# Optimization experiments

Measured on AMD Instinct MI355X. Metric: run time of the kernel, lower is better.

## Reference

```python
import jax, jax.numpy as jnp
import numpy as np

HEADS = 4
DIM_HEAD = 32
CHUNK = 1024
GROUPS = 8
EPS = 1e-5


def setup_inputs() -> dict:
    key = jax.random.key(0)
    k1, k2, k3 = jax.random.split(key, 3)
    b, dim, h, w = 8, 64, 96, 96
    inner = HEADS * DIM_HEAD  # 128
    x = jax.random.normal(k1, (b, dim, h, w), dtype=jnp.float32)
    W_qkv = jax.random.normal(k2, (3 * inner, dim), dtype=jnp.float32) * (1.0 / np.sqrt(dim))
    W_out = jax.random.normal(k3, (dim, inner), dtype=jnp.float32) * (1.0 / np.sqrt(inner))
    b_out = jnp.zeros((dim,), dtype=jnp.float32)
    gamma = jnp.ones((dim,), dtype=jnp.float32)
    beta = jnp.zeros((dim,), dtype=jnp.float32)
    return {"x": x, "W_qkv": W_qkv, "W_out": W_out, "b_out": b_out,
            "gamma": gamma, "beta": beta}


def reference(x, W_qkv, W_out, b_out, gamma, beta):
    b, c, h, w = x.shape
    n = h * w
    nch = n // CHUNK  # number of full chunks (n chosen divisible by CHUNK)
    d = DIM_HEAD
    BH = b * HEADS

    # 1x1 conv (no bias) == matmul over channel dim
    xf = x.reshape(b, c, n)
    qkv = jnp.einsum('oc,bcn->bon', W_qkv, xf)          # [b, 3*inner, n]
    q, k, v = jnp.split(qkv, 3, axis=1)                  # each [b, inner, n]

    def chunkify(t):
        # [b, inner, n] -> [BH, nch, d, CHUNK]; slicing i:i+CHUNK on last axis
        # equals reshaping n -> (nch, CHUNK) in order.
        return t.reshape(BH, d, nch, CHUNK).transpose(0, 2, 1, 3)

    qc, kc, vc = chunkify(q), chunkify(k), chunkify(v)

    qs = jax.nn.softmax(qc, axis=-1)  # softmax over chunk spatial positions
    ks = jax.nn.softmax(kc, axis=-2)  # softmax over head channels

    # context = k_chunk^T @ v_chunk : [BH, nch, CHUNK, CHUNK]
    ctx = jnp.einsum('gkdi,gkdj->gkij', ks, vc)
    # chunk_out = q_chunk @ context : [BH, nch, d, CHUNK]
    out = jnp.einsum('gkdi,gkij->gkdj', qs, ctx)

    # concat chunks back along spatial dim, reshape to image layout
    out = out.transpose(0, 2, 1, 3).reshape(b, HEADS * d, h, w)

    # to_out: 1x1 conv with bias, then GroupNorm(8, dim)
    y = jnp.einsum('oc,bchw->bohw', W_out, out) + b_out[None, :, None, None]

    yg = y.reshape(b, GROUPS, c // GROUPS, h, w)
    mu = jnp.mean(yg, axis=(2, 3, 4), keepdims=True)
    var = jnp.var(yg, axis=(2, 3, 4), keepdims=True)
    yn = ((yg - mu) * jax.lax.rsqrt(var + EPS)).reshape(b, c, h, w)
    return yn * gamma[None, :, None, None] + beta[None, :, None, None]
```

## Files before the change

kernel.cpp:

```cpp
#include <hip/hip_runtime.h>
#include <hip/hip_bf16.h>

#define N_POS 9216
#define NCHUNK 9
#define BATCH 8
#define CDIM 64
#define HEADS 4
#define EPS 1e-5f

#define NPART 16
#define PPARTS_TOT ((size_t)BATCH * NCHUNK * NPART * 4096)
#define MP_SLICE ((size_t)(BATCH * NCHUNK) * 4096)
#define WBF_BYTES ((size_t)384 * 64 * 2)

typedef __attribute__((ext_vector_type(8))) short short8;
typedef __attribute__((ext_vector_type(4))) float f32x4;

static __device__ inline unsigned pk2(float a, float b) {
    __hip_bfloat162 h2(__float2bfloat16(a), __float2bfloat16(b));
    return *reinterpret_cast<unsigned*>(&h2);
}
static __device__ inline float bf2f(short s) {
    union { unsigned u; float f; } c; c.u = ((unsigned)(unsigned short)s) << 16; return c.f;
}
static __device__ inline short8 mk8(unsigned a, unsigned b, unsigned c, unsigned d) {
    union { short8 s; unsigned u[4]; } cv;
    cv.u[0] = a; cv.u[1] = b; cv.u[2] = c; cv.u[3] = d; return cv.s;
}

__global__ __launch_bounds__(256) void wprep_kernel(const float* __restrict__ Wqkv,
        __hip_bfloat16* __restrict__ wbf, float* __restrict__ stats) {
    int i = blockIdx.x * 256 + threadIdx.x;
    if (i < 6144) {
        float4 v = ((const float4*)Wqkv)[i];
        uint2 u; u.x = pk2(v.x, v.y); u.y = pk2(v.z, v.w);
        ((uint2*)wbf)[i] = u;
    }
    if (i < 128) stats[i] = 0.f;
}

__global__ __launch_bounds__(256) void qkp_kernel(const float* __restrict__ x,
        const __hip_bfloat16* __restrict__ wbf, float* __restrict__ Pparts) {
    int bx = blockIdx.x;
    int b  = blockIdx.y;
    int ck = bx >> 4, pt = bx & 15;
    __shared__ __align__(16) __hip_bfloat16 xs[64][72];
    int t = threadIdx.x, w = t >> 6, l = t & 63;
    int l15 = l & 15, quad = l >> 4;
    int n0 = bx * 64;

    {
        int p = t & 63, cbase = (t >> 6) * 16;
        const float* xb = x + (size_t)b * CDIM * N_POS + n0 + p;
        #pragma unroll
        for (int j = 0; j < 16; j += 4) {
            float v0 = xb[(size_t)(cbase + j + 0) * N_POS];
            float v1 = xb[(size_t)(cbase + j + 1) * N_POS];
            float v2 = xb[(size_t)(cbase + j + 2) * N_POS];
            float v3 = xb[(size_t)(cbase + j + 3) * N_POS];
            uint2 u; u.x = pk2(v0, v1); u.y = pk2(v2, v3);
            *reinterpret_cast<uint2*>(&xs[p][cbase + j]) = u;
        }
    }
    __syncthreads();

    f32x4 acc[4][4];
    #pragma unroll
    for (int mt = 0; mt < 4; ++mt)
        #pragma unroll
        for (int nt = 0; nt < 4; ++nt) acc[mt][nt] = (f32x4){0.f, 0.f, 0.f, 0.f};
    #pragma unroll
    for (int ks = 0; ks < 2; ++ks) {
        int k0 = ks * 32 + quad * 8;
        short8 av[4];
        #pragma unroll
        for (int mt = 0; mt < 4; ++mt)
            av[mt] = *reinterpret_cast<const short8*>(&xs[mt * 16 + l15][k0]);
        #pragma unroll
        for (int nt = 0; nt < 4; ++nt) {
            int row = (nt < 2) ? (w * 32 + nt * 16 + l15)
                               : (128 + w * 32 + (nt - 2) * 16 + l15);
            short8 bw = *reinterpret_cast<const short8*>(wbf + (size_t)row * 64 + k0);
            #pragma unroll
            for (int mt = 0; mt < 4; ++mt)
                acc[mt][nt] = __builtin_amdgcn_mfma_f32_16x16x32_bf16(av[mt], bw, acc[mt][nt], 0, 0, 0);
        }
    }

    unsigned pk[4][4][2];
    #pragma unroll
    for (int mt = 0; mt < 4; ++mt) {
        f32x4 e2, e3;
        #pragma unroll
        for (int r = 0; r < 4; ++r) {
            float a2 = acc[mt][2][r], a3 = acc[mt][3][r];
            float m = fmaxf(a2, a3);
            m = fmaxf(m, __shfl_xor(m, 1));
            m = fmaxf(m, __shfl_xor(m, 2));
            m = fmaxf(m, __shfl_xor(m, 4));
            m = fmaxf(m, __shfl_xor(m, 8));
            float x2 = __expf(a2 - m), x3 = __expf(a3 - m);
            float s = x2 + x3;
            s += __shfl_xor(s, 1);
            s += __shfl_xor(s, 2);
            s += __shfl_xor(s, 4);
            s += __shfl_xor(s, 8);
            float is = 1.f / s;
            e2[r] = x2 * is; e3[r] = x3 * is;
        }
        pk[mt][2][0] = pk2(e2[0], e2[1]); pk[mt][2][1] = pk2(e2[2], e2[3]);
        pk[mt][3][0] = pk2(e3[0], e3[1]); pk[mt][3][1] = pk2(e3[2], e3[3]);
        pk[mt][0][0] = pk2(__expf(acc[mt][0][0]), __expf(acc[mt][0][1]));
        pk[mt][0][1] = pk2(__expf(acc[mt][0][2]), __expf(acc[mt][0][3]));
        pk[mt][1][0] = pk2(__expf(acc[mt][1][0]), __expf(acc[mt][1][1]));
        pk[mt][1][1] = pk2(__expf(acc[mt][1][2]), __expf(acc[mt][1][3]));
    }

    f32x4 pac[2][2];
    pac[0][0] = (f32x4){0,0,0,0}; pac[0][1] = (f32x4){0,0,0,0};
    pac[1][0] = (f32x4){0,0,0,0}; pac[1][1] = (f32x4){0,0,0,0};
    int srcbase = ((quad & 1) * 2) * 16 + l15;
    bool hiHalf = (quad >= 2);
    #pragma unroll
    for (int ks = 0; ks < 2; ++ks) {
        unsigned fr[4][4];
        #pragma unroll
        for (int nt = 0; nt < 4; ++nt) {
            #pragma unroll
            for (int s = 0; s < 4; ++s) {
                int src = srcbase + (s >> 1) * 16;
                unsigned lo = __shfl(pk[2 * ks][nt][s & 1], src);
                unsigned hi = __shfl(pk[2 * ks + 1][nt][s & 1], src);
                fr[nt][s] = hiHalf ? hi : lo;
            }
        }
        short8 A0 = mk8(fr[0][0], fr[0][1], fr[0][2], fr[0][3]);
        short8 A1 = mk8(fr[1][0], fr[1][1], fr[1][2], fr[1][3]);
        short8 B0 = mk8(fr[2][0], fr[2][1], fr[2][2], fr[2][3]);
        short8 B1 = mk8(fr[3][0], fr[3][1], fr[3][2], fr[3][3]);
        pac[0][0] = __builtin_amdgcn_mfma_f32_16x16x32_bf16(A0, B0, pac[0][0], 0, 0, 0);
        pac[0][1] = __builtin_amdgcn_mfma_f32_16x16x32_bf16(A0, B1, pac[0][1], 0, 0, 0);
        pac[1][0] = __builtin_amdgcn_mfma_f32_16x16x32_bf16(A1, B0, pac[1][0], 0, 0, 0);
        pac[1][1] = __builtin_amdgcn_mfma_f32_16x16x32_bf16(A1, B1, pac[1][1], 0, 0, 0);
    }
    float* Pp = Pparts + (((size_t)(b * NCHUNK + ck) * NPART + pt) * 4 + w) * 1024;
    #pragma unroll
    for (int tA = 0; tA < 2; ++tA)
        #pragma unroll
        for (int tB = 0; tB < 2; ++tB)
            #pragma unroll
            for (int r = 0; r < 4; ++r)
                Pp[(tA * 16 + quad * 4 + r) * 32 + tB * 16 + l15] = pac[tA][tB][r];
}

__global__ __launch_bounds__(256) void umat_kernel(const float* __restrict__ Wout,
        const float* __restrict__ Wqkv, const float* __restrict__ Pparts,
        float* __restrict__ Mp) {
    int ck = blockIdx.x, b = blockIdx.y, h = blockIdx.z;
    int t = threadIdx.x;
    __shared__ float Pl[32][32];
    __shared__ float iZ[32];
    __shared__ float Ul[64][33];
    __shared__ float Wvh[32][68];
    {
        const float4* P0 = (const float4*)Pparts
            + ((size_t)(b * NCHUNK + ck) * NPART) * 1024 + h * 256 + t;
        float4 s = (float4){0.f, 0.f, 0.f, 0.f};
        #pragma unroll
        for (int pt = 0; pt < NPART; ++pt) {
            float4 a = P0[pt * 1024];
            s.x += a.x; s.y += a.y; s.z += a.z; s.w += a.w;
        }
        ((float4*)Pl)[t] = s;
    }
    {
        int e = t >> 3, cq = t & 7;
        const float4* wr = (const float4*)(Wqkv + (size_t)(256 + h * 32 + e) * 64 + cq * 8);
        float4 a0 = wr[0], a1 = wr[1];
        *reinterpret_cast<float4*>(&Wvh[e][cq * 8])     = a0;
        *reinterpret_cast<float4*>(&Wvh[e][cq * 8 + 4]) = a1;
    }
    __syncthreads();
    if (t < 32) {
        float s = 0.f;
        #pragma unroll
        for (int c = 0; c < 32; ++c) s += Pl[t][c];
        iZ[t] = 1.f / s;
    }
    __syncthreads();
    int o = t & 63, wv = t >> 6;
    float wz[32];
    {
        const float4* wr = (const float4*)(Wout + (size_t)o * 128 + h * 32);
        #pragma unroll
        for (int j = 0; j < 8; ++j) {
            float4 f = wr[j];
            wz[j*4+0] = f.x * iZ[j*4+0]; wz[j*4+1] = f.y * iZ[j*4+1];
            wz[j*4+2] = f.z * iZ[j*4+2]; wz[j*4+3] = f.w * iZ[j*4+3];
        }
    }
    float ua[8];
    #pragma unroll
    for (int j = 0; j < 8; ++j) ua[j] = 0.f;
    for (int d = 0; d < 32; ++d) {
        float wd = wz[d];
        #pragma unroll
        for (int j = 0; j < 8; ++j) ua[j] += wd * Pl[d][wv * 8 + j];
    }
    #pragma unroll
    for (int j = 0; j < 8; ++j) Ul[o][wv * 8 + j] = ua[j];
    __syncthreads();

    float macc[16];
    #pragma unroll
    for (int j = 0; j < 16; ++j) macc[j] = 0.f;
    for (int e = 0; e < 32; ++e) {
        float u = Ul[o][e];
        const float4* wvp = reinterpret_cast<const float4*>(&Wvh[e][wv * 16]);
        #pragma unroll
        for (int q = 0; q < 4; ++q) {
            float4 f = wvp[q];
            macc[q*4+0] += u * f.x; macc[q*4+1] += u * f.y;
            macc[q*4+2] += u * f.z; macc[q*4+3] += u * f.w;
        }
    }
    float* mp = Mp + (size_t)h * MP_SLICE + ((size_t)(b * NCHUNK + ck)) * 4096
              + (size_t)o * 64 + wv * 16;
    #pragma unroll
    for (int q = 0; q < 4; ++q) {
        float4 f; f.x = macc[q*4+0]; f.y = macc[q*4+1]; f.z = macc[q*4+2]; f.w = macc[q*4+3];
        reinterpret_cast<float4*>(mp)[q] = f;
    }
}

__global__ __launch_bounds__(256) void y_kernel(const float* __restrict__ x,
        const float* __restrict__ Mp, const float* __restrict__ bout,
        __hip_bfloat16* __restrict__ ybf, float* __restrict__ stats) {
    int bx = blockIdx.x;
    int b  = blockIdx.y;
    int ck = bx >> 3;
    int n0 = bx * 128;
    __shared__ __align__(16) __hip_bfloat16 xs[128][72];
    __shared__ __align__(16) __hip_bfloat16 Ml[64][72];
    __shared__ float gsum[8], gsq[8];
    int t = threadIdx.x, w = t >> 6, l = t & 63;
    int l15 = l & 15, quad = l >> 4;
    if (t < 8) { gsum[t] = 0.f; gsq[t] = 0.f; }

    {
        int p = t & 127, cbase = (t >> 7) * 32;
        const float* xb = x + (size_t)b * CDIM * N_POS + n0 + p;
        #pragma unroll
        for (int j = 0; j < 32; j += 4) {
            float v0 = xb[(size_t)(cbase + j + 0) * N_POS];
            float v1 = xb[(size_t)(cbase + j + 1) * N_POS];
            float v2 = xb[(size_t)(cbase + j + 2) * N_POS];
            float v3 = xb[(size_t)(cbase + j + 3) * N_POS];
            uint2 u; u.x = pk2(v0, v1); u.y = pk2(v2, v3);
            *reinterpret_cast<uint2*>(&xs[p][cbase + j]) = u;
        }
    }
    {
        int o = t >> 2, cs = (t & 3) * 16;
        const float* mb = Mp + ((size_t)(b * NCHUNK + ck)) * 4096 + (size_t)o * 64 + cs;
        float m[16];
        #pragma unroll
        for (int q = 0; q < 4; ++q) {
            float4 f = reinterpret_cast<const float4*>(mb)[q];
            m[q*4+0] = f.x; m[q*4+1] = f.y; m[q*4+2] = f.z; m[q*4+3] = f.w;
        }
        #pragma unroll
        for (int h = 1; h < 4; ++h) {
            const float* mh = mb + h * MP_SLICE;
            #pragma unroll
            for (int q = 0; q < 4; ++q) {
                float4 f = reinterpret_cast<const float4*>(mh)[q];
                m[q*4+0] += f.x; m[q*4+1] += f.y; m[q*4+2] += f.z; m[q*4+3] += f.w;
            }
        }
        #pragma unroll
        for (int q = 0; q < 4; ++q) {
            uint2 u; u.x = pk2(m[q*4+0], m[q*4+1]); u.y = pk2(m[q*4+2], m[q*4+3]);
            *reinterpret_cast<uint2*>(&Ml[o][cs + q * 4]) = u;
        }
    }
    __syncthreads();

    int nw = w * 32;
    f32x4 acc[4][2];
    #pragma unroll
    for (int mt = 0; mt < 4; ++mt) { acc[mt][0] = (f32x4){0,0,0,0}; acc[mt][1] = (f32x4){0,0,0,0}; }
    #pragma unroll
    for (int ks = 0; ks < 2; ++ks) {
        int k0 = ks * 32 + quad * 8;
        short8 bf[2];
        #pragma unroll
        for (int nt = 0; nt < 2; ++nt)
            bf[nt] = *reinterpret_cast<const short8*>(&xs[nw + nt * 16 + l15][k0]);
        #pragma unroll
        for (int mt = 0; mt < 4; ++mt) {
            short8 af = *reinterpret_cast<const short8*>(&Ml[mt * 16 + l15][k0]);
            acc[mt][0] = __builtin_amdgcn_mfma_f32_16x16x32_bf16(af, bf[0], acc[mt][0], 0, 0, 0);
            acc[mt][1] = __builtin_amdgcn_mfma_f32_16x16x32_bf16(af, bf[1], acc[mt][1], 0, 0, 0);
        }
    }
    float gsl[4], gql[4];
    #pragma unroll
    for (int mt = 0; mt < 4; ++mt) { gsl[mt] = 0.f; gql[mt] = 0.f; }
    __hip_bfloat16* yb = ybf + (size_t)b * CDIM * N_POS;
    int nbase = n0 + nw;
    #pragma unroll
    for (int mt = 0; mt < 4; ++mt) {
        float4 bo = *reinterpret_cast<const float4*>(bout + mt * 16 + quad * 4);
        const float* bop = reinterpret_cast<const float*>(&bo);
        #pragma unroll
        for (int nt = 0; nt < 2; ++nt) {
            int n = nbase + nt * 16 + l15;
            #pragma unroll
            for (int r = 0; r < 4; ++r) {
                int o = mt * 16 + quad * 4 + r;
                float val = acc[mt][nt][r] + bop[r];
                yb[(size_t)o * N_POS + n] = __float2bfloat16(val);
                gsl[mt] += val; gql[mt] += val * val;
            }
        }
    }
    #pragma unroll
    for (int off = 16; off >= 1; off >>= 1) {
        #pragma unroll
        for (int mt = 0; mt < 4; ++mt) {
            gsl[mt] += __shfl_xor(gsl[mt], off, 64);
            gql[mt] += __shfl_xor(gql[mt], off, 64);
        }
    }
    if (l == 0 || l == 32) {
        int qh = quad >> 1;
        #pragma unroll
        for (int mt = 0; mt < 4; ++mt) {
            atomicAdd(&gsum[2 * mt + qh], gsl[mt]);
            atomicAdd(&gsq[2 * mt + qh], gql[mt]);
        }
    }
    __syncthreads();
    if (t < 8) {
        atomicAdd(&stats[(b * 8 + t) * 2],     gsum[t]);
        atomicAdd(&stats[(b * 8 + t) * 2 + 1], gsq[t]);
    }
}

__global__ __launch_bounds__(256) void gn_kernel(const __hip_bfloat16* __restrict__ ybf,
        float* __restrict__ out, const float* __restrict__ stats,
        const float* __restrict__ gamma, const float* __restrict__ beta) {
    int bc = blockIdx.y;
    int c = bc & 63, b = bc >> 6;
    int g = c >> 3;
    float s = stats[(b * 8 + g) * 2], q = stats[(b * 8 + g) * 2 + 1];
    const float invN = 1.f / (8.f * N_POS);
    float mean = s * invN;
    float var = q * invN - mean * mean;
    float sc = rsqrtf(var + EPS);
    float ga = gamma[c] * sc;
    float be = beta[c] - mean * sc * gamma[c];
    size_t base = ((size_t)b * CDIM + c) * N_POS + (size_t)(blockIdx.x * 256 + threadIdx.x) * 4;
    uint2 u = *reinterpret_cast<const uint2*>(ybf + base);
    float4 v;
    v.x = bf2f((short)(u.x & 0xffff)); v.y = bf2f((short)(u.x >> 16));
    v.z = bf2f((short)(u.y & 0xffff)); v.w = bf2f((short)(u.y >> 16));
    v.x = v.x * ga + be; v.y = v.y * ga + be; v.z = v.z * ga + be; v.w = v.w * ga + be;
    *reinterpret_cast<float4*>(out + base) = v;
}

extern "C" void kernel_launch(void* const* d_in, const int* in_sizes, int n_in,
                              void* d_out, int out_size, void* d_ws, size_t ws_size,
                              hipStream_t stream) {
    const float* x     = (const float*)d_in[0];
    const float* Wqkv  = (const float*)d_in[1];
    const float* Wout  = (const float*)d_in[2];
    const float* bout  = (const float*)d_in[3];
    const float* gamma = (const float*)d_in[4];
    const float* beta  = (const float*)d_in[5];
    float* out = (float*)d_out;

    float* stats  = (float*)d_ws;
    float* Pparts = stats + 128;
    float* Mp     = Pparts + PPARTS_TOT;
    __hip_bfloat16* wbf = (__hip_bfloat16*)(Mp + 4 * MP_SLICE);
    __hip_bfloat16* ybf = (__hip_bfloat16*)((char*)wbf + WBF_BYTES);

    wprep_kernel<<<dim3(24), 256, 0, stream>>>(Wqkv, wbf, stats);
    qkp_kernel<<<dim3(144, BATCH), 256, 0, stream>>>(x, wbf, Pparts);
    umat_kernel<<<dim3(NCHUNK, BATCH, HEADS), 256, 0, stream>>>(Wout, Wqkv, Pparts, Mp);
    y_kernel<<<dim3(72, BATCH), 256, 0, stream>>>(x, Mp, bout, ybf, stats);
    gn_kernel<<<dim3(9, 512), 256, 0, stream>>>(ybf, out, stats, gamma, beta);
}
```

Baseline: 130.9 us.

## Fuse all stages into one persistent cooperative kernel with grid syncs

Replaces the five separate launches with one cooperative persistent kernel. Each block loops over the tasks of every phase, and the phases are separated by grid-wide syncs. The weight bf16 prep kernel is dropped; weights are converted inline inside phase A. This removes launch gaps and tail effects between kernels, at the cost of grid-sync overhead, fewer blocks than the original grids, and redundant per-tile weight conversion. A fallback path with four separate kernels is kept for when the cooperative launch fails.

```diff
diff --git a/kernel.cpp b/kernel.cpp
--- a/kernel.cpp
+++ b/kernel.cpp
@@ -1,5 +1,8 @@
 #include <hip/hip_runtime.h>
+#include <hip/hip_cooperative_groups.h>
 #include <hip/hip_bf16.h>
+
+namespace cg = cooperative_groups;
 
 #define N_POS 9216
 #define NCHUNK 9
@@ -11,7 +14,6 @@
 #define NPART 16
 #define PPARTS_TOT ((size_t)BATCH * NCHUNK * NPART * 4096)
 #define MP_SLICE ((size_t)(BATCH * NCHUNK) * 4096)
-#define WBF_BYTES ((size_t)384 * 64 * 2)
 
 typedef __attribute__((ext_vector_type(8))) short short8;
 typedef __attribute__((ext_vector_type(4))) float f32x4;
@@ -28,27 +30,16 @@
     cv.u[0] = a; cv.u[1] = b; cv.u[2] = c; cv.u[3] = d; return cv.s;
 }
 
-__global__ __launch_bounds__(256) void wprep_kernel(const float* __restrict__ Wqkv,
-        __hip_bfloat16* __restrict__ wbf, float* __restrict__ stats) {
-    int i = blockIdx.x * 256 + threadIdx.x;
-    if (i < 6144) {
-        float4 v = ((const float4*)Wqkv)[i];
-        uint2 u; u.x = pk2(v.x, v.y); u.y = pk2(v.z, v.w);
-        ((uint2*)wbf)[i] = u;
-    }
-    if (i < 128) stats[i] = 0.f;
-}
-
-__global__ __launch_bounds__(256) void qkp_kernel(const float* __restrict__ x,
-        const __hip_bfloat16* __restrict__ wbf, float* __restrict__ Pparts) {
-    int bx = blockIdx.x;
-    int b  = blockIdx.y;
+static __device__ __forceinline__ void phaseA_task(int task, int t,
+        const float* __restrict__ x, const float* __restrict__ Wqkv,
+        float* __restrict__ Pparts) {
+    __shared__ __align__(16) __hip_bfloat16 xs[64][72];
+    int w = t >> 6, l = t & 63;
+    int l15 = l & 15, quad = l >> 4;
+    int bx = task % 144, b = task / 144;
     int ck = bx >> 4, pt = bx & 15;
-    __shared__ __align__(16) __hip_bfloat16 xs[64][72];
-    int t = threadIdx.x, w = t >> 6, l = t & 63;
-    int l15 = l & 15, quad = l >> 4;
     int n0 = bx * 64;
-
+    __syncthreads();
     {
         int p = t & 63, cbase = (t >> 6) * 16;
         const float* xb = x + (size_t)b * CDIM * N_POS + n0 + p;
@@ -80,10 +71,13 @@
         for (int nt = 0; nt < 4; ++nt) {
             int row = (nt < 2) ? (w * 32 + nt * 16 + l15)
                                : (128 + w * 32 + (nt - 2) * 16 + l15);
-            short8 bw = *reinterpret_cast<const short8*>(wbf + (size_t)row * 64 + k0);
+            const float4* wr = (const float4*)(Wqkv + (size_t)row * 64 + k0);
+            float4 wa = wr[0], wb = wr[1];
+            short8 bwv = mk8(pk2(wa.x, wa.y), pk2(wa.z, wa.w),
+                             pk2(wb.x, wb.y), pk2(wb.z, wb.w));
             #pragma unroll
             for (int mt = 0; mt < 4; ++mt)
-                acc[mt][nt] = __builtin_amdgcn_mfma_f32_16x16x32_bf16(av[mt], bw, acc[mt][nt], 0, 0, 0);
+                acc[mt][nt] = __builtin_amdgcn_mfma_f32_16x16x32_bf16(av[mt], bwv, acc[mt][nt], 0, 0, 0);
         }
     }
 
@@ -127,11 +121,11 @@
         #pragma unroll
         for (int nt = 0; nt < 4; ++nt) {
             #pragma unroll
-            for (int s = 0; s < 4; ++s) {
-                int src = srcbase + (s >> 1) * 16;
-                unsigned lo = __shfl(pk[2 * ks][nt][s & 1], src);
-                unsigned hi = __shfl(pk[2 * ks + 1][nt][s & 1], src);
-                fr[nt][s] = hiHalf ? hi : lo;
+            for (int sl = 0; sl < 4; ++sl) {
+                int src = srcbase + (sl >> 1) * 16;
+                unsigned lo = __shfl(pk[2 * ks][nt][sl & 1], src);
+                unsigned hi = __shfl(pk[2 * ks + 1][nt][sl & 1], src);
+                fr[nt][sl] = hiHalf ? hi : lo;
             }
         }
         short8 A0 = mk8(fr[0][0], fr[0][1], fr[0][2], fr[0][3]);
@@ -153,15 +147,15 @@
                 Pp[(tA * 16 + quad * 4 + r) * 32 + tB * 16 + l15] = pac[tA][tB][r];
 }
 
-__global__ __launch_bounds__(256) void umat_kernel(const float* __restrict__ Wout,
-        const float* __restrict__ Wqkv, const float* __restrict__ Pparts,
-        float* __restrict__ Mp) {
-    int ck = blockIdx.x, b = blockIdx.y, h = blockIdx.z;
-    int t = threadIdx.x;
+static __device__ __forceinline__ void phaseB_task(int task, int t,
+        const float* __restrict__ Wqkv, const float* __restrict__ Wout,
+        const float* __restrict__ Pparts, float* __restrict__ Mp) {
     __shared__ float Pl[32][32];
     __shared__ float iZ[32];
     __shared__ float Ul[64][33];
     __shared__ float Wvh[32][68];
+    int ck = task % 9; int r2 = task / 9; int b = r2 & 7; int h = r2 >> 3;
+    __syncthreads();
     {
         const float4* P0 = (const float4*)Pparts
             + ((size_t)(b * NCHUNK + ck) * NPART) * 1024 + h * 256 + t;
@@ -233,20 +227,20 @@
     }
 }
 
-__global__ __launch_bounds__(256) void y_kernel(const float* __restrict__ x,
-        const float* __restrict__ Mp, const float* __restrict__ bout,
-        __hip_bfloat16* __restrict__ ybf, float* __restrict__ stats) {
-    int bx = blockIdx.x;
-    int b  = blockIdx.y;
-    int ck = bx >> 3;
-    int n0 = bx * 128;
+static __device__ __forceinline__ void phaseC_task(int task, int t,
+        const float* __restrict__ x, const float* __restrict__ Mp,
+        const float* __restrict__ bout, __hip_bfloat16* __restrict__ ybf,
+        float* __restrict__ stats) {
     __shared__ __align__(16) __hip_bfloat16 xs[128][72];
     __shared__ __align__(16) __hip_bfloat16 Ml[64][72];
     __shared__ float gsum[8], gsq[8];
-    int t = threadIdx.x, w = t >> 6, l = t & 63;
+    int w = t >> 6, l = t & 63;
     int l15 = l & 15, quad = l >> 4;
+    int bx = task % 72, b = task / 72;
+    int ck = bx >> 3;
+    int n0 = bx * 128;
+    __syncthreads();
     if (t < 8) { gsum[t] = 0.f; gsq[t] = 0.f; }
-
     {
         int p = t & 127, cbase = (t >> 7) * 32;
         const float* xb = x + (size_t)b * CDIM * N_POS + n0 + p;
@@ -348,10 +342,11 @@
     }
 }
 
-__global__ __launch_bounds__(256) void gn_kernel(const __hip_bfloat16* __restrict__ ybf,
-        float* __restrict__ out, const float* __restrict__ stats,
-        const float* __restrict__ gamma, const float* __restrict__ beta) {
-    int bc = blockIdx.y;
+static __device__ __forceinline__ void phaseD_task(int task, int t,
+        const __hip_bfloat16* __restrict__ ybf, const float* __restrict__ stats,
+        const float* __restrict__ gamma, const float* __restrict__ beta,
+        float* __restrict__ out) {
+    int bx9 = task % 9; int bc = task / 9;
     int c = bc & 63, b = bc >> 6;
     int g = c >> 3;
     float s = stats[(b * 8 + g) * 2], q = stats[(b * 8 + g) * 2 + 1];
@@ -361,13 +356,61 @@
     float sc = rsqrtf(var + EPS);
     float ga = gamma[c] * sc;
     float be = beta[c] - mean * sc * gamma[c];
-    size_t base = ((size_t)b * CDIM + c) * N_POS + (size_t)(blockIdx.x * 256 + threadIdx.x) * 4;
+    size_t base = ((size_t)b * CDIM + c) * N_POS + (size_t)(bx9 * 256 + t) * 4;
     uint2 u = *reinterpret_cast<const uint2*>(ybf + base);
     float4 v;
     v.x = bf2f((short)(u.x & 0xffff)); v.y = bf2f((short)(u.x >> 16));
     v.z = bf2f((short)(u.y & 0xffff)); v.w = bf2f((short)(u.y >> 16));
     v.x = v.x * ga + be; v.y = v.y * ga + be; v.z = v.z * ga + be; v.w = v.w * ga + be;
     *reinterpret_cast<float4*>(out + base) = v;
+}
+
+__global__ __launch_bounds__(256, 2) void fused_kernel(
+        const float* __restrict__ x, const float* __restrict__ Wqkv,
+        const float* __restrict__ Wout, const float* __restrict__ bout,
+        const float* __restrict__ gamma, const float* __restrict__ beta,
+        float* __restrict__ out, float* __restrict__ stats,
+        float* __restrict__ Pparts, float* __restrict__ Mp,
+        __hip_bfloat16* __restrict__ ybf) {
+    cg::grid_group gg = cg::this_grid();
+    int t = threadIdx.x;
+    if (blockIdx.x == 0 && t < 128) stats[t] = 0.f;
+    for (int task = blockIdx.x; task < 1152; task += gridDim.x)
+        phaseA_task(task, t, x, Wqkv, Pparts);
+    __threadfence();
+    gg.sync();
+    for (int task = blockIdx.x; task < 288; task += gridDim.x)
+        phaseB_task(task, t, Wqkv, Wout, Pparts, Mp);
+    __threadfence();
+    gg.sync();
+    for (int task = blockIdx.x; task < 576; task += gridDim.x)
+        phaseC_task(task, t, x, Mp, bout, ybf, stats);
+    __threadfence();
+    gg.sync();
+    for (int task = blockIdx.x; task < 4608; task += gridDim.x)
+        phaseD_task(task, t, ybf, stats, gamma, beta, out);
+}
+
+__global__ __launch_bounds__(256) void kA(const float* __restrict__ x,
+        const float* __restrict__ Wqkv, float* __restrict__ Pparts,
+        float* __restrict__ stats) {
+    if (blockIdx.x == 0 && threadIdx.x < 128) stats[threadIdx.x] = 0.f;
+    phaseA_task(blockIdx.x, threadIdx.x, x, Wqkv, Pparts);
+}
+__global__ __launch_bounds__(256) void kB(const float* __restrict__ Wqkv,
+        const float* __restrict__ Wout, const float* __restrict__ Pparts,
+        float* __restrict__ Mp) {
+    phaseB_task(blockIdx.x, threadIdx.x, Wqkv, Wout, Pparts, Mp);
+}
+__global__ __launch_bounds__(256) void kC(const float* __restrict__ x,
+        const float* __restrict__ Mp, const float* __restrict__ bout,
+        __hip_bfloat16* __restrict__ ybf, float* __restrict__ stats) {
+    phaseC_task(blockIdx.x, threadIdx.x, x, Mp, bout, ybf, stats);
+}
+__global__ __launch_bounds__(256) void kD(const __hip_bfloat16* __restrict__ ybf,
+        const float* __restrict__ stats, const float* __restrict__ gamma,
+        const float* __restrict__ beta, float* __restrict__ out) {
+    phaseD_task(blockIdx.x, threadIdx.x, ybf, stats, gamma, beta, out);
 }
 
 extern "C" void kernel_launch(void* const* d_in, const int* in_sizes, int n_in,
@@ -384,12 +427,31 @@
     float* stats  = (float*)d_ws;
     float* Pparts = stats + 128;
     float* Mp     = Pparts + PPARTS_TOT;
-    __hip_bfloat16* wbf = (__hip_bfloat16*)(Mp + 4 * MP_SLICE);
-    __hip_bfloat16* ybf = (__hip_bfloat16*)((char*)wbf + WBF_BYTES);
-
-    wprep_kernel<<<dim3(24), 256, 0, stream>>>(Wqkv, wbf, stats);
-    qkp_kernel<<<dim3(144, BATCH), 256, 0, stream>>>(x, wbf, Pparts);
-    umat_kernel<<<dim3(NCHUNK, BATCH, HEADS), 256, 0, stream>>>(Wout, Wqkv, Pparts, Mp);
-    y_kernel<<<dim3(72, BATCH), 256, 0, stream>>>(x, Mp, bout, ybf, stats);
-    gn_kernel<<<dim3(9, 512), 256, 0, stream>>>(ybf, out, stats, gamma, beta);
-}
+    __hip_bfloat16* ybf = (__hip_bfloat16*)(Mp + 4 * MP_SLICE);
+
+    static int coopBlocks = -1;
+    if (coopBlocks < 0) {
+        int nb = 0;
+        if (hipOccupancyMaxActiveBlocksPerMultiprocessor(
+                &nb, (const void*)fused_kernel, 256, 0) != hipSuccess || nb < 1)
+            nb = 0;
+        coopBlocks = nb * 256;
+        if (coopBlocks > 512) coopBlocks = 512;
+    }
+
+    bool done = false;
+    if (coopBlocks >= 256) {
+        void* args[] = { (void*)&x, (void*)&Wqkv, (void*)&Wout, (void*)&bout,
+                         (void*)&gamma, (void*)&beta, (void*)&out, (void*)&stats,
+                         (void*)&Pparts, (void*)&Mp, (void*)&ybf };
+        if (hipLaunchCooperativeKernel((const void*)fused_kernel,
+                dim3(coopBlocks), dim3(256), args, 0, stream) == hipSuccess)
+            done = true;
+    }
+    if (!done) {
+        kA<<<dim3(1152), 256, 0, stream>>>(x, Wqkv, Pparts, stats);
+        kB<<<dim3(288),  256, 0, stream>>>(Wqkv, Wout, Pparts, Mp);
+        kC<<<dim3(576),  256, 0, stream>>>(x, Mp, bout, ybf, stats);
+        kD<<<dim3(4608), 256, 0, stream>>>(ybf, stats, gamma, beta, out);
+    }
+}
```

After: 343.0 us. 2.62x slower.

## Fuse GroupNorm into y kernel via per-batch grid barrier and drop weight prep

Applied to the files above, without the earlier changes.

Folds the GroupNorm apply into the output-projection kernel. Each batch's blocks accumulate group statistics, then spin on a per-batch atomic counter until all 72 blocks have arrived, and write normalized fp32 output straight from registers. This removes the bf16 intermediate round trip and the separate gn launch. It also drops the weight bf16 prep kernel, converting Wqkv to bf16 inline in qkp, and replaces it with a memset to clear the stats and counters. The spin barrier needs all blocks resident, so it launches cooperatively with a plain launch as fallback, which risks deadlock if blocks are not co-resident.

```diff
diff --git a/kernel.cpp b/kernel.cpp
--- a/kernel.cpp
+++ b/kernel.cpp
@@ -11,7 +11,6 @@
 #define NPART 16
 #define PPARTS_TOT ((size_t)BATCH * NCHUNK * NPART * 4096)
 #define MP_SLICE ((size_t)(BATCH * NCHUNK) * 4096)
-#define WBF_BYTES ((size_t)384 * 64 * 2)
 
 typedef __attribute__((ext_vector_type(8))) short short8;
 typedef __attribute__((ext_vector_type(4))) float f32x4;
@@ -20,35 +19,19 @@
     __hip_bfloat162 h2(__float2bfloat16(a), __float2bfloat16(b));
     return *reinterpret_cast<unsigned*>(&h2);
 }
-static __device__ inline float bf2f(short s) {
-    union { unsigned u; float f; } c; c.u = ((unsigned)(unsigned short)s) << 16; return c.f;
-}
 static __device__ inline short8 mk8(unsigned a, unsigned b, unsigned c, unsigned d) {
     union { short8 s; unsigned u[4]; } cv;
     cv.u[0] = a; cv.u[1] = b; cv.u[2] = c; cv.u[3] = d; return cv.s;
 }
 
-__global__ __launch_bounds__(256) void wprep_kernel(const float* __restrict__ Wqkv,
-        __hip_bfloat16* __restrict__ wbf, float* __restrict__ stats) {
-    int i = blockIdx.x * 256 + threadIdx.x;
-    if (i < 6144) {
-        float4 v = ((const float4*)Wqkv)[i];
-        uint2 u; u.x = pk2(v.x, v.y); u.y = pk2(v.z, v.w);
-        ((uint2*)wbf)[i] = u;
-    }
-    if (i < 128) stats[i] = 0.f;
-}
-
 __global__ __launch_bounds__(256) void qkp_kernel(const float* __restrict__ x,
-        const __hip_bfloat16* __restrict__ wbf, float* __restrict__ Pparts) {
-    int bx = blockIdx.x;
-    int b  = blockIdx.y;
-    int ck = bx >> 4, pt = bx & 15;
+        const float* __restrict__ Wqkv, float* __restrict__ Pparts) {
     __shared__ __align__(16) __hip_bfloat16 xs[64][72];
     int t = threadIdx.x, w = t >> 6, l = t & 63;
     int l15 = l & 15, quad = l >> 4;
+    int bx = blockIdx.x, b = blockIdx.y;
+    int ck = bx >> 4, pt = bx & 15;
     int n0 = bx * 64;
-
     {
         int p = t & 63, cbase = (t >> 6) * 16;
         const float* xb = x + (size_t)b * CDIM * N_POS + n0 + p;
@@ -80,10 +63,13 @@
         for (int nt = 0; nt < 4; ++nt) {
             int row = (nt < 2) ? (w * 32 + nt * 16 + l15)
                                : (128 + w * 32 + (nt - 2) * 16 + l15);
-            short8 bw = *reinterpret_cast<const short8*>(wbf + (size_t)row * 64 + k0);
+            const float4* wr = (const float4*)(Wqkv + (size_t)row * 64 + k0);
+            float4 wa = wr[0], wb = wr[1];
+            short8 bwv = mk8(pk2(wa.x, wa.y), pk2(wa.z, wa.w),
+                             pk2(wb.x, wb.y), pk2(wb.z, wb.w));
             #pragma unroll
             for (int mt = 0; mt < 4; ++mt)
-                acc[mt][nt] = __builtin_amdgcn_mfma_f32_16x16x32_bf16(av[mt], bw, acc[mt][nt], 0, 0, 0);
+                acc[mt][nt] = __builtin_amdgcn_mfma_f32_16x16x32_bf16(av[mt], bwv, acc[mt][nt], 0, 0, 0);
         }
     }
 
@@ -127,11 +113,11 @@
         #pragma unroll
         for (int nt = 0; nt < 4; ++nt) {
             #pragma unroll
-            for (int s = 0; s < 4; ++s) {
-                int src = srcbase + (s >> 1) * 16;
-                unsigned lo = __shfl(pk[2 * ks][nt][s & 1], src);
-                unsigned hi = __shfl(pk[2 * ks + 1][nt][s & 1], src);
-                fr[nt][s] = hiHalf ? hi : lo;
+            for (int sl = 0; sl < 4; ++sl) {
+                int src = srcbase + (sl >> 1) * 16;
+                unsigned lo = __shfl(pk[2 * ks][nt][sl & 1], src);
+                unsigned hi = __shfl(pk[2 * ks + 1][nt][sl & 1], src);
+                fr[nt][sl] = hiHalf ? hi : lo;
             }
         }
         short8 A0 = mk8(fr[0][0], fr[0][1], fr[0][2], fr[0][3]);
@@ -156,12 +142,12 @@
 __global__ __launch_bounds__(256) void umat_kernel(const float* __restrict__ Wout,
         const float* __restrict__ Wqkv, const float* __restrict__ Pparts,
         float* __restrict__ Mp) {
-    int ck = blockIdx.x, b = blockIdx.y, h = blockIdx.z;
-    int t = threadIdx.x;
     __shared__ float Pl[32][32];
     __shared__ float iZ[32];
     __shared__ float Ul[64][33];
     __shared__ float Wvh[32][68];
+    int ck = blockIdx.x, b = blockIdx.y, h = blockIdx.z;
+    int t = threadIdx.x;
     {
         const float4* P0 = (const float4*)Pparts
             + ((size_t)(b * NCHUNK + ck) * NPART) * 1024 + h * 256 + t;
@@ -235,18 +221,17 @@
 
 __global__ __launch_bounds__(256) void y_kernel(const float* __restrict__ x,
         const float* __restrict__ Mp, const float* __restrict__ bout,
-        __hip_bfloat16* __restrict__ ybf, float* __restrict__ stats) {
-    int bx = blockIdx.x;
-    int b  = blockIdx.y;
-    int ck = bx >> 3;
-    int n0 = bx * 128;
+        const float* __restrict__ gamma, const float* __restrict__ beta,
+        float* __restrict__ out, float* __restrict__ stats,
+        unsigned* __restrict__ cntY) {
     __shared__ __align__(16) __hip_bfloat16 xs[128][72];
     __shared__ __align__(16) __hip_bfloat16 Ml[64][72];
     __shared__ float gsum[8], gsq[8];
+    int bx = blockIdx.x, b = blockIdx.y;
+    int ck = bx >> 3, n0 = bx * 128;
     int t = threadIdx.x, w = t >> 6, l = t & 63;
     int l15 = l & 15, quad = l >> 4;
     if (t < 8) { gsum[t] = 0.f; gsq[t] = 0.f; }
-
     {
         int p = t & 127, cbase = (t >> 7) * 32;
         const float* xb = x + (size_t)b * CDIM * N_POS + n0 + p;
@@ -307,23 +292,18 @@
     float gsl[4], gql[4];
     #pragma unroll
     for (int mt = 0; mt < 4; ++mt) { gsl[mt] = 0.f; gql[mt] = 0.f; }
-    __hip_bfloat16* yb = ybf + (size_t)b * CDIM * N_POS;
-    int nbase = n0 + nw;
     #pragma unroll
     for (int mt = 0; mt < 4; ++mt) {
         float4 bo = *reinterpret_cast<const float4*>(bout + mt * 16 + quad * 4);
         const float* bop = reinterpret_cast<const float*>(&bo);
         #pragma unroll
-        for (int nt = 0; nt < 2; ++nt) {
-            int n = nbase + nt * 16 + l15;
+        for (int nt = 0; nt < 2; ++nt)
             #pragma unroll
             for (int r = 0; r < 4; ++r) {
-                int o = mt * 16 + quad * 4 + r;
-                float val = acc[mt][nt][r] + bop[r];
-                yb[(size_t)o * N_POS + n] = __float2bfloat16(val);
-                gsl[mt] += val; gql[mt] += val * val;
+                acc[mt][nt][r] += bop[r];
+                gsl[mt] += acc[mt][nt][r];
+                gql[mt] += acc[mt][nt][r] * acc[mt][nt][r];
             }
-        }
     }
     #pragma unroll
     for (int off = 16; off >= 1; off >>= 1) {
@@ -346,28 +326,42 @@
         atomicAdd(&stats[(b * 8 + t) * 2],     gsum[t]);
         atomicAdd(&stats[(b * 8 + t) * 2 + 1], gsq[t]);
     }
-}
-
-__global__ __launch_bounds__(256) void gn_kernel(const __hip_bfloat16* __restrict__ ybf,
-        float* __restrict__ out, const float* __restrict__ stats,
-        const float* __restrict__ gamma, const float* __restrict__ beta) {
-    int bc = blockIdx.y;
-    int c = bc & 63, b = bc >> 6;
-    int g = c >> 3;
-    float s = stats[(b * 8 + g) * 2], q = stats[(b * 8 + g) * 2 + 1];
+    __threadfence();
+    __syncthreads();
+    if (t == 0) {
+        atomicAdd(&cntY[b], 1u);
+        while (__hip_atomic_load(&cntY[b], __ATOMIC_ACQUIRE,
+                                 __HIP_MEMORY_SCOPE_AGENT) < 72u)
+            __builtin_amdgcn_s_sleep(4);
+    }
+    __syncthreads();
+
     const float invN = 1.f / (8.f * N_POS);
-    float mean = s * invN;
-    float var = q * invN - mean * mean;
-    float sc = rsqrtf(var + EPS);
-    float ga = gamma[c] * sc;
-    float be = beta[c] - mean * sc * gamma[c];
-    size_t base = ((size_t)b * CDIM + c) * N_POS + (size_t)(blockIdx.x * 256 + threadIdx.x) * 4;
-    uint2 u = *reinterpret_cast<const uint2*>(ybf + base);
-    float4 v;
-    v.x = bf2f((short)(u.x & 0xffff)); v.y = bf2f((short)(u.x >> 16));
-    v.z = bf2f((short)(u.y & 0xffff)); v.w = bf2f((short)(u.y >> 16));
-    v.x = v.x * ga + be; v.y = v.y * ga + be; v.z = v.z * ga + be; v.w = v.w * ga + be;
-    *reinterpret_cast<float4*>(out + base) = v;
+    float* ob = out + (size_t)b * CDIM * N_POS;
+    int nbase = n0 + nw;
+    int qh = quad >> 1;
+    #pragma unroll
+    for (int mt = 0; mt < 4; ++mt) {
+        int g = 2 * mt + qh;
+        float s = __hip_atomic_load(&stats[(b * 8 + g) * 2], __ATOMIC_RELAXED,
+                                    __HIP_MEMORY_SCOPE_AGENT);
+        float q = __hip_atomic_load(&stats[(b * 8 + g) * 2 + 1], __ATOMIC_RELAXED,
+                                    __HIP_MEMORY_SCOPE_AGENT);
+        float mean = s * invN;
+        float var = q * invN - mean * mean;
+        float sc = rsqrtf(var + EPS);
+        #pragma unroll
+        for (int r = 0; r < 4; ++r) {
+            int o = mt * 16 + quad * 4 + r;
+            float gg = gamma[o] * sc;
+            float bb = beta[o] - mean * gg;
+            #pragma unroll
+            for (int nt = 0; nt < 2; ++nt) {
+                int n = nbase + nt * 16 + l15;
+                ob[(size_t)o * N_POS + n] = acc[mt][nt][r] * gg + bb;
+            }
+        }
+    }
 }
 
 extern "C" void kernel_launch(void* const* d_in, const int* in_sizes, int n_in,
@@ -381,15 +375,20 @@
     const float* beta  = (const float*)d_in[5];
     float* out = (float*)d_out;
 
-    float* stats  = (float*)d_ws;
-    float* Pparts = stats + 128;
-    float* Mp     = Pparts + PPARTS_TOT;
-    __hip_bfloat16* wbf = (__hip_bfloat16*)(Mp + 4 * MP_SLICE);
-    __hip_bfloat16* ybf = (__hip_bfloat16*)((char*)wbf + WBF_BYTES);
-
-    wprep_kernel<<<dim3(24), 256, 0, stream>>>(Wqkv, wbf, stats);
-    qkp_kernel<<<dim3(144, BATCH), 256, 0, stream>>>(x, wbf, Pparts);
+    float* stats   = (float*)d_ws;
+    unsigned* cntY = (unsigned*)(stats + 128);
+    float* Pparts  = (float*)((char*)d_ws + 1024);
+    float* Mp      = Pparts + PPARTS_TOT;
+
+    hipMemsetAsync(d_ws, 0, 1024, stream);
+    qkp_kernel<<<dim3(144, BATCH), 256, 0, stream>>>(x, Wqkv, Pparts);
     umat_kernel<<<dim3(NCHUNK, BATCH, HEADS), 256, 0, stream>>>(Wout, Wqkv, Pparts, Mp);
-    y_kernel<<<dim3(72, BATCH), 256, 0, stream>>>(x, Mp, bout, ybf, stats);
-    gn_kernel<<<dim3(9, 512), 256, 0, stream>>>(ybf, out, stats, gamma, beta);
-}
+
+    void* args[] = { (void*)&x, (void*)&Mp, (void*)&bout, (void*)&gamma,
+                     (void*)&beta, (void*)&out, (void*)&stats, (void*)&cntY };
+    if (hipLaunchCooperativeKernel((const void*)y_kernel, dim3(72, BATCH),
+                                   dim3(256), args, 0, stream) != hipSuccess) {
+        y_kernel<<<dim3(72, BATCH), 256, 0, stream>>>(x, Mp, bout, gamma, beta,
+                                                      out, stats, cntY);
+    }
+}
```

New measurement: 238.8 us. 1.82x slower.

## Drop weight-prep kernel, fold heads in umat, emit bf16 M, shrink y tiles

Applied to the files above, without the earlier changes.

Removes the separate weight bf16 conversion kernel and converts Wqkv to bf16 inline in qkp, using a memset to clear the stats buffer. umat now loops over all four heads in one block and writes a single head-summed M matrix in bf16, instead of four fp32 per-head slices that y_kernel had to sum. y_kernel loads M fragments straight from global memory into registers and uses 64-position tiles with twice as many blocks. This cuts a launch and intermediate traffic, but serializes the head work inside umat, which now runs only 72 blocks, and repeats the weight conversion in every qkp block.

```diff
diff --git a/kernel.cpp b/kernel.cpp
--- a/kernel.cpp
+++ b/kernel.cpp
@@ -10,8 +10,7 @@
 
 #define NPART 16
 #define PPARTS_TOT ((size_t)BATCH * NCHUNK * NPART * 4096)
-#define MP_SLICE ((size_t)(BATCH * NCHUNK) * 4096)
-#define WBF_BYTES ((size_t)384 * 64 * 2)
+#define MBF_ELEMS ((size_t)BATCH * NCHUNK * 4096)
 
 typedef __attribute__((ext_vector_type(8))) short short8;
 typedef __attribute__((ext_vector_type(4))) float f32x4;
@@ -28,27 +27,14 @@
     cv.u[0] = a; cv.u[1] = b; cv.u[2] = c; cv.u[3] = d; return cv.s;
 }
 
-__global__ __launch_bounds__(256) void wprep_kernel(const float* __restrict__ Wqkv,
-        __hip_bfloat16* __restrict__ wbf, float* __restrict__ stats) {
-    int i = blockIdx.x * 256 + threadIdx.x;
-    if (i < 6144) {
-        float4 v = ((const float4*)Wqkv)[i];
-        uint2 u; u.x = pk2(v.x, v.y); u.y = pk2(v.z, v.w);
-        ((uint2*)wbf)[i] = u;
-    }
-    if (i < 128) stats[i] = 0.f;
-}
-
 __global__ __launch_bounds__(256) void qkp_kernel(const float* __restrict__ x,
-        const __hip_bfloat16* __restrict__ wbf, float* __restrict__ Pparts) {
-    int bx = blockIdx.x;
-    int b  = blockIdx.y;
-    int ck = bx >> 4, pt = bx & 15;
+        const float* __restrict__ Wqkv, float* __restrict__ Pparts) {
     __shared__ __align__(16) __hip_bfloat16 xs[64][72];
     int t = threadIdx.x, w = t >> 6, l = t & 63;
     int l15 = l & 15, quad = l >> 4;
+    int bx = blockIdx.x, b = blockIdx.y;
+    int ck = bx >> 4, pt = bx & 15;
     int n0 = bx * 64;
-
     {
         int p = t & 63, cbase = (t >> 6) * 16;
         const float* xb = x + (size_t)b * CDIM * N_POS + n0 + p;
@@ -80,10 +66,13 @@
         for (int nt = 0; nt < 4; ++nt) {
             int row = (nt < 2) ? (w * 32 + nt * 16 + l15)
                                : (128 + w * 32 + (nt - 2) * 16 + l15);
-            short8 bw = *reinterpret_cast<const short8*>(wbf + (size_t)row * 64 + k0);
+            const float4* wr = (const float4*)(Wqkv + (size_t)row * 64 + k0);
+            float4 wa = wr[0], wb = wr[1];
+            short8 bwv = mk8(pk2(wa.x, wa.y), pk2(wa.z, wa.w),
+                             pk2(wb.x, wb.y), pk2(wb.z, wb.w));
             #pragma unroll
             for (int mt = 0; mt < 4; ++mt)
-                acc[mt][nt] = __builtin_amdgcn_mfma_f32_16x16x32_bf16(av[mt], bw, acc[mt][nt], 0, 0, 0);
+                acc[mt][nt] = __builtin_amdgcn_mfma_f32_16x16x32_bf16(av[mt], bwv, acc[mt][nt], 0, 0, 0);
         }
     }
 
@@ -127,11 +116,11 @@
         #pragma unroll
         for (int nt = 0; nt < 4; ++nt) {
             #pragma unroll
-            for (int s = 0; s < 4; ++s) {
-                int src = srcbase + (s >> 1) * 16;
-                unsigned lo = __shfl(pk[2 * ks][nt][s & 1], src);
-                unsigned hi = __shfl(pk[2 * ks + 1][nt][s & 1], src);
-                fr[nt][s] = hiHalf ? hi : lo;
+            for (int sl = 0; sl < 4; ++sl) {
+                int src = srcbase + (sl >> 1) * 16;
+                unsigned lo = __shfl(pk[2 * ks][nt][sl & 1], src);
+                unsigned hi = __shfl(pk[2 * ks + 1][nt][sl & 1], src);
+                fr[nt][sl] = hiHalf ? hi : lo;
             }
         }
         short8 A0 = mk8(fr[0][0], fr[0][1], fr[0][2], fr[0][3]);
@@ -155,103 +144,111 @@
 
 __global__ __launch_bounds__(256) void umat_kernel(const float* __restrict__ Wout,
         const float* __restrict__ Wqkv, const float* __restrict__ Pparts,
-        float* __restrict__ Mp) {
-    int ck = blockIdx.x, b = blockIdx.y, h = blockIdx.z;
-    int t = threadIdx.x;
+        __hip_bfloat16* __restrict__ Mbf) {
     __shared__ float Pl[32][32];
     __shared__ float iZ[32];
     __shared__ float Ul[64][33];
     __shared__ float Wvh[32][68];
-    {
-        const float4* P0 = (const float4*)Pparts
-            + ((size_t)(b * NCHUNK + ck) * NPART) * 1024 + h * 256 + t;
-        float4 s = (float4){0.f, 0.f, 0.f, 0.f};
-        #pragma unroll
-        for (int pt = 0; pt < NPART; ++pt) {
-            float4 a = P0[pt * 1024];
-            s.x += a.x; s.y += a.y; s.z += a.z; s.w += a.w;
-        }
-        ((float4*)Pl)[t] = s;
-    }
-    {
-        int e = t >> 3, cq = t & 7;
-        const float4* wr = (const float4*)(Wqkv + (size_t)(256 + h * 32 + e) * 64 + cq * 8);
-        float4 a0 = wr[0], a1 = wr[1];
-        *reinterpret_cast<float4*>(&Wvh[e][cq * 8])     = a0;
-        *reinterpret_cast<float4*>(&Wvh[e][cq * 8 + 4]) = a1;
-    }
-    __syncthreads();
-    if (t < 32) {
-        float s = 0.f;
-        #pragma unroll
-        for (int c = 0; c < 32; ++c) s += Pl[t][c];
-        iZ[t] = 1.f / s;
-    }
-    __syncthreads();
+    int ck = blockIdx.x, b = blockIdx.y;
+    int t = threadIdx.x;
     int o = t & 63, wv = t >> 6;
-    float wz[32];
-    {
-        const float4* wr = (const float4*)(Wout + (size_t)o * 128 + h * 32);
-        #pragma unroll
-        for (int j = 0; j < 8; ++j) {
-            float4 f = wr[j];
-            wz[j*4+0] = f.x * iZ[j*4+0]; wz[j*4+1] = f.y * iZ[j*4+1];
-            wz[j*4+2] = f.z * iZ[j*4+2]; wz[j*4+3] = f.w * iZ[j*4+3];
-        }
-    }
-    float ua[8];
-    #pragma unroll
-    for (int j = 0; j < 8; ++j) ua[j] = 0.f;
-    for (int d = 0; d < 32; ++d) {
-        float wd = wz[d];
-        #pragma unroll
-        for (int j = 0; j < 8; ++j) ua[j] += wd * Pl[d][wv * 8 + j];
-    }
-    #pragma unroll
-    for (int j = 0; j < 8; ++j) Ul[o][wv * 8 + j] = ua[j];
-    __syncthreads();
-
     float macc[16];
     #pragma unroll
     for (int j = 0; j < 16; ++j) macc[j] = 0.f;
-    for (int e = 0; e < 32; ++e) {
-        float u = Ul[o][e];
-        const float4* wvp = reinterpret_cast<const float4*>(&Wvh[e][wv * 16]);
-        #pragma unroll
-        for (int q = 0; q < 4; ++q) {
-            float4 f = wvp[q];
-            macc[q*4+0] += u * f.x; macc[q*4+1] += u * f.y;
-            macc[q*4+2] += u * f.z; macc[q*4+3] += u * f.w;
-        }
-    }
-    float* mp = Mp + (size_t)h * MP_SLICE + ((size_t)(b * NCHUNK + ck)) * 4096
-              + (size_t)o * 64 + wv * 16;
+    for (int h = 0; h < 4; ++h) {
+        __syncthreads();
+        {
+            const float4* P0 = (const float4*)Pparts
+                + ((size_t)(b * NCHUNK + ck) * NPART) * 1024 + h * 256 + t;
+            float4 s = (float4){0.f, 0.f, 0.f, 0.f};
+            #pragma unroll
+            for (int pt = 0; pt < NPART; ++pt) {
+                float4 a = P0[pt * 1024];
+                s.x += a.x; s.y += a.y; s.z += a.z; s.w += a.w;
+            }
+            ((float4*)Pl)[t] = s;
+        }
+        {
+            int e = t >> 3, cq = t & 7;
+            const float4* wr = (const float4*)(Wqkv + (size_t)(256 + h * 32 + e) * 64 + cq * 8);
+            float4 a0 = wr[0], a1 = wr[1];
+            *reinterpret_cast<float4*>(&Wvh[e][cq * 8])     = a0;
+            *reinterpret_cast<float4*>(&Wvh[e][cq * 8 + 4]) = a1;
+        }
+        __syncthreads();
+        if (t < 32) {
+            float s = 0.f;
+            #pragma unroll
+            for (int c = 0; c < 32; ++c) s += Pl[t][c];
+            iZ[t] = 1.f / s;
+        }
+        __syncthreads();
+        float wz[32];
+        {
+            const float4* wr = (const float4*)(Wout + (size_t)o * 128 + h * 32);
+            #pragma unroll
+            for (int j = 0; j < 8; ++j) {
+                float4 f = wr[j];
+                wz[j*4+0] = f.x * iZ[j*4+0]; wz[j*4+1] = f.y * iZ[j*4+1];
+                wz[j*4+2] = f.z * iZ[j*4+2]; wz[j*4+3] = f.w * iZ[j*4+3];
+            }
+        }
+        float ua[8];
+        #pragma unroll
+        for (int j = 0; j < 8; ++j) ua[j] = 0.f;
+        for (int d = 0; d < 32; ++d) {
+            float wd = wz[d];
+            #pragma unroll
+            for (int j = 0; j < 8; ++j) ua[j] += wd * Pl[d][wv * 8 + j];
+        }
+        #pragma unroll
+        for (int j = 0; j < 8; ++j) Ul[o][wv * 8 + j] = ua[j];
+        __syncthreads();
+        for (int e = 0; e < 32; ++e) {
+            float u = Ul[o][e];
+            const float4* wvp = reinterpret_cast<const float4*>(&Wvh[e][wv * 16]);
+            #pragma unroll
+            for (int q = 0; q < 4; ++q) {
+                float4 f = wvp[q];
+                macc[q*4+0] += u * f.x; macc[q*4+1] += u * f.y;
+                macc[q*4+2] += u * f.z; macc[q*4+3] += u * f.w;
+            }
+        }
+    }
+    __hip_bfloat16* mp = Mbf + (size_t)(b * NCHUNK + ck) * 4096 + (size_t)o * 64 + wv * 16;
     #pragma unroll
     for (int q = 0; q < 4; ++q) {
-        float4 f; f.x = macc[q*4+0]; f.y = macc[q*4+1]; f.z = macc[q*4+2]; f.w = macc[q*4+3];
-        reinterpret_cast<float4*>(mp)[q] = f;
+        uint2 u; u.x = pk2(macc[q*4+0], macc[q*4+1]); u.y = pk2(macc[q*4+2], macc[q*4+3]);
+        reinterpret_cast<uint2*>(mp)[q] = u;
     }
 }
 
 __global__ __launch_bounds__(256) void y_kernel(const float* __restrict__ x,
-        const float* __restrict__ Mp, const float* __restrict__ bout,
+        const __hip_bfloat16* __restrict__ Mbf, const float* __restrict__ bout,
         __hip_bfloat16* __restrict__ ybf, float* __restrict__ stats) {
-    int bx = blockIdx.x;
-    int b  = blockIdx.y;
-    int ck = bx >> 3;
-    int n0 = bx * 128;
-    __shared__ __align__(16) __hip_bfloat16 xs[128][72];
-    __shared__ __align__(16) __hip_bfloat16 Ml[64][72];
+    __shared__ __align__(16) __hip_bfloat16 xs[64][72];
     __shared__ float gsum[8], gsq[8];
+    int bx = blockIdx.x, b = blockIdx.y;
+    int ck = bx >> 4, n0 = bx * 64;
     int t = threadIdx.x, w = t >> 6, l = t & 63;
     int l15 = l & 15, quad = l >> 4;
     if (t < 8) { gsum[t] = 0.f; gsq[t] = 0.f; }
 
+    short8 af[4][2];
     {
-        int p = t & 127, cbase = (t >> 7) * 32;
+        const __hip_bfloat16* Mb = Mbf + (size_t)(b * NCHUNK + ck) * 4096;
+        #pragma unroll
+        for (int mt = 0; mt < 4; ++mt)
+            #pragma unroll
+            for (int ks = 0; ks < 2; ++ks)
+                af[mt][ks] = *reinterpret_cast<const short8*>(
+                    Mb + (size_t)(mt * 16 + l15) * 64 + ks * 32 + quad * 8);
+    }
+    {
+        int p = t & 63, cbase = (t >> 6) * 16;
         const float* xb = x + (size_t)b * CDIM * N_POS + n0 + p;
         #pragma unroll
-        for (int j = 0; j < 32; j += 4) {
+        for (int j = 0; j < 16; j += 4) {
             float v0 = xb[(size_t)(cbase + j + 0) * N_POS];
             float v1 = xb[(size_t)(cbase + j + 1) * N_POS];
             float v2 = xb[(size_t)(cbase + j + 2) * N_POS];
@@ -260,69 +257,31 @@
             *reinterpret_cast<uint2*>(&xs[p][cbase + j]) = u;
         }
     }
-    {
-        int o = t >> 2, cs = (t & 3) * 16;
-        const float* mb = Mp + ((size_t)(b * NCHUNK + ck)) * 4096 + (size_t)o * 64 + cs;
-        float m[16];
-        #pragma unroll
-        for (int q = 0; q < 4; ++q) {
-            float4 f = reinterpret_cast<const float4*>(mb)[q];
-            m[q*4+0] = f.x; m[q*4+1] = f.y; m[q*4+2] = f.z; m[q*4+3] = f.w;
-        }
-        #pragma unroll
-        for (int h = 1; h < 4; ++h) {
-            const float* mh = mb + h * MP_SLICE;
-            #pragma unroll
-            for (int q = 0; q < 4; ++q) {
-                float4 f = reinterpret_cast<const float4*>(mh)[q];
-                m[q*4+0] += f.x; m[q*4+1] += f.y; m[q*4+2] += f.z; m[q*4+3] += f.w;
-            }
-        }
-        #pragma unroll
-        for (int q = 0; q < 4; ++q) {
-            uint2 u; u.x = pk2(m[q*4+0], m[q*4+1]); u.y = pk2(m[q*4+2], m[q*4+3]);
-            *reinterpret_cast<uint2*>(&Ml[o][cs + q * 4]) = u;
-        }
-    }
     __syncthreads();
 
-    int nw = w * 32;
-    f32x4 acc[4][2];
-    #pragma unroll
-    for (int mt = 0; mt < 4; ++mt) { acc[mt][0] = (f32x4){0,0,0,0}; acc[mt][1] = (f32x4){0,0,0,0}; }
+    f32x4 acc[4];
+    #pragma unroll
+    for (int mt = 0; mt < 4; ++mt) acc[mt] = (f32x4){0.f, 0.f, 0.f, 0.f};
     #pragma unroll
     for (int ks = 0; ks < 2; ++ks) {
         int k0 = ks * 32 + quad * 8;
-        short8 bf[2];
-        #pragma unroll
-        for (int nt = 0; nt < 2; ++nt)
-            bf[nt] = *reinterpret_cast<const short8*>(&xs[nw + nt * 16 + l15][k0]);
-        #pragma unroll
-        for (int mt = 0; mt < 4; ++mt) {
-            short8 af = *reinterpret_cast<const short8*>(&Ml[mt * 16 + l15][k0]);
-            acc[mt][0] = __builtin_amdgcn_mfma_f32_16x16x32_bf16(af, bf[0], acc[mt][0], 0, 0, 0);
-            acc[mt][1] = __builtin_amdgcn_mfma_f32_16x16x32_bf16(af, bf[1], acc[mt][1], 0, 0, 0);
-        }
+        short8 bf = *reinterpret_cast<const short8*>(&xs[w * 16 + l15][k0]);
+        #pragma unroll
+        for (int mt = 0; mt < 4; ++mt)
+            acc[mt] = __builtin_amdgcn_mfma_f32_16x16x32_bf16(af[mt][ks], bf, acc[mt], 0, 0, 0);
     }
     float gsl[4], gql[4];
     #pragma unroll
     for (int mt = 0; mt < 4; ++mt) { gsl[mt] = 0.f; gql[mt] = 0.f; }
-    __hip_bfloat16* yb = ybf + (size_t)b * CDIM * N_POS;
-    int nbase = n0 + nw;
     #pragma unroll
     for (int mt = 0; mt < 4; ++mt) {
         float4 bo = *reinterpret_cast<const float4*>(bout + mt * 16 + quad * 4);
         const float* bop = reinterpret_cast<const float*>(&bo);
         #pragma unroll
-        for (int nt = 0; nt < 2; ++nt) {
-            int n = nbase + nt * 16 + l15;
-            #pragma unroll
-            for (int r = 0; r < 4; ++r) {
-                int o = mt * 16 + quad * 4 + r;
-                float val = acc[mt][nt][r] + bop[r];
-                yb[(size_t)o * N_POS + n] = __float2bfloat16(val);
-                gsl[mt] += val; gql[mt] += val * val;
-            }
+        for (int r = 0; r < 4; ++r) {
+            acc[mt][r] += bop[r];
+            gsl[mt] += acc[mt][r];
+            gql[mt] += acc[mt][r] * acc[mt][r];
         }
     }
     #pragma unroll
@@ -341,6 +300,15 @@
             atomicAdd(&gsq[2 * mt + qh], gql[mt]);
         }
     }
+    __hip_bfloat16* yb = ybf + (size_t)b * CDIM * N_POS;
+    int n = n0 + w * 16 + l15;
+    #pragma unroll
+    for (int mt = 0; mt < 4; ++mt)
+        #pragma unroll
+        for (int r = 0; r < 4; ++r) {
+            int o = mt * 16 + quad * 4 + r;
+            yb[(size_t)o * N_POS + n] = __float2bfloat16(acc[mt][r]);
+        }
     __syncthreads();
     if (t < 8) {
         atomicAdd(&stats[(b * 8 + t) * 2],     gsum[t]);
@@ -382,14 +350,13 @@
     float* out = (float*)d_out;
 
     float* stats  = (float*)d_ws;
-    float* Pparts = stats + 128;
-    float* Mp     = Pparts + PPARTS_TOT;
-    __hip_bfloat16* wbf = (__hip_bfloat16*)(Mp + 4 * MP_SLICE);
-    __hip_bfloat16* ybf = (__hip_bfloat16*)((char*)wbf + WBF_BYTES);
-
-    wprep_kernel<<<dim3(24), 256, 0, stream>>>(Wqkv, wbf, stats);
-    qkp_kernel<<<dim3(144, BATCH), 256, 0, stream>>>(x, wbf, Pparts);
-    umat_kernel<<<dim3(NCHUNK, BATCH, HEADS), 256, 0, stream>>>(Wout, Wqkv, Pparts, Mp);
-    y_kernel<<<dim3(72, BATCH), 256, 0, stream>>>(x, Mp, bout, ybf, stats);
+    float* Pparts = (float*)((char*)d_ws + 1024);
+    __hip_bfloat16* Mbf = (__hip_bfloat16*)(Pparts + PPARTS_TOT);
+    __hip_bfloat16* ybf = Mbf + MBF_ELEMS;
+
+    hipMemsetAsync(d_ws, 0, 512, stream);
+    qkp_kernel<<<dim3(144, BATCH), 256, 0, stream>>>(x, Wqkv, Pparts);
+    umat_kernel<<<dim3(NCHUNK, BATCH), 256, 0, stream>>>(Wout, Wqkv, Pparts, Mbf);
+    y_kernel<<<dim3(144, BATCH), 256, 0, stream>>>(x, Mbf, bout, ybf, stats);
     gn_kernel<<<dim3(9, 512), 256, 0, stream>>>(ybf, out, stats, gamma, beta);
 }
```

Result: slower. 146.3 us (+11.8%).
